# Kernel tuning notes

Measured on AMD Instinct MI355X. Metric: run time of the kernel, lower is better.

The kernel has to match this reference:

```python
import jax, jax.numpy as jnp
import numpy as np

B, S, H, D = 2, 4096, 16, 128
TILE = 128
T = S // TILE          # 32 tiles
TOPK = 7               # anchor-selected tiles per query tile (local tile appended -> 8)
DM = H * D
NEG = -1e10


def setup_inputs() -> dict:
    key = jax.random.key(0)
    ks = jax.random.split(key, 6)
    x = jax.random.normal(ks[0], (B, S, DM), dtype=jnp.float32)
    wq = jax.random.normal(ks[1], (DM, H * D), dtype=jnp.float32) * 0.02
    wk = jax.random.normal(ks[2], (DM, H * D), dtype=jnp.float32) * 0.02
    wv = jax.random.normal(ks[3], (DM, H * D), dtype=jnp.float32) * 0.02
    wo = jax.random.normal(ks[4], (H * D, DM), dtype=jnp.float32) * 0.02
    # RoPE tables (real/imag of freqs_cis), LLaMA-style
    inv_freq = 1.0 / (10000.0 ** (np.arange(0, D, 2, dtype=np.float32) / D))  # [D/2]
    t = np.arange(S, dtype=np.float32)
    freqs = np.outer(t, inv_freq)  # [S, D/2]
    cos = jnp.asarray(np.cos(freqs), dtype=jnp.float32)
    sin = jnp.asarray(np.sin(freqs), dtype=jnp.float32)
    anchor_indices = jax.random.randint(ks[5], (B, H, T, TOPK), 0, T, dtype=jnp.int32)
    return {"x": x, "wq": wq, "wk": wk, "wv": wv, "wo": wo,
            "cos": cos, "sin": sin, "anchor_indices": anchor_indices}


def _apply_rope(q, k, cos, sin):
    # q,k: [B,H,S,D]; cos,sin: [S,D/2]
    cos_f = jnp.concatenate([cos, cos], axis=-1)[None, None]  # [1,1,S,D]
    sin_f = jnp.concatenate([sin, sin], axis=-1)[None, None]

    def rot_half(x):
        h = x.shape[-1] // 2
        return jnp.concatenate([-x[..., h:], x[..., :h]], axis=-1)

    return q * cos_f + rot_half(q) * sin_f, k * cos_f + rot_half(k) * sin_f


def reference(x, wq, wk, wv, wo, cos, sin, anchor_indices):
    b, s, _ = x.shape
    h = anchor_indices.shape[1]
    t = anchor_indices.shape[2]
    tile = s // t
    d = wq.shape[1] // h

    q = (x @ wq).reshape(b, s, h, d).transpose(0, 2, 1, 3)  # [B,H,S,D]
    k = (x @ wk).reshape(b, s, h, d).transpose(0, 2, 1, 3)
    v = (x @ wv).reshape(b, s, h, d).transpose(0, 2, 1, 3)
    q, k = _apply_rope(q, k, cos, sin)

    # append local tile to anchor-selected tiles -> [B,H,T,K+1]
    local = jnp.broadcast_to(jnp.arange(t, dtype=jnp.int32)[None, None, :, None], (b, h, t, 1))
    tile_sel = jnp.concatenate([anchor_indices, local], axis=-1)
    # token indices of gathered tiles: [B,H,T,(K+1)*tile]
    offs = jnp.arange(tile, dtype=jnp.int32)[None, None, None, None, :]
    tok_idx = (tile_sel[..., None] * tile + offs)
    sparse_len = tile_sel.shape[-1] * tile
    flat_idx = jnp.clip(tok_idx.reshape(b, h, t, sparse_len), 0, s - 1)

    # gather K/V tiles: [B,H,T,L,D]
    gid = flat_idx.reshape(b, h, t * sparse_len)
    k_sp = jnp.take_along_axis(k, gid[..., None], axis=2).reshape(b, h, t, sparse_len, d)
    v_sp = jnp.take_along_axis(v, gid[..., None], axis=2).reshape(b, h, t, sparse_len, d)

    q_t = q.reshape(b, h, t, tile, d)
    logits = jnp.einsum('bhtqd,bhtkd->bhtqk', q_t, k_sp) / jnp.sqrt(jnp.float32(d))

    # causal future-mask within gathered set
    q_pos = jnp.arange(s, dtype=jnp.int32).reshape(t, tile)
    fut = flat_idx[:, :, :, None, :] > q_pos[None, None, :, :, None]  # [B,H,T,tile,L]
    logits = jnp.where(fut, NEG, logits)
    weights = jax.nn.softmax(logits, axis=-1)
    all_masked = jnp.all(fut, axis=-1, keepdims=True)
    weights = jnp.where(all_masked, 0.0, weights)
    weights = jnp.where(jnp.isnan(weights), 0.0, weights)

    out = jnp.einsum('bhtqk,bhtkd->bhtqd', weights, v_sp)
    out = out.reshape(b, h, s, d).transpose(0, 2, 1, 3).reshape(b, s, h * d)
    return out @ wo
```

## Files before the change

kernel.cpp:

```cpp
#include <hip/hip_runtime.h>
#include <hip/hip_bf16.h>


typedef __bf16 bf16_t;
using bf16x8 = __attribute__((ext_vector_type(8))) __bf16;
using bf16x4 = __attribute__((ext_vector_type(4))) __bf16;
using f32x4  = __attribute__((ext_vector_type(4))) float;

typedef const __attribute__((address_space(1))) void* gas_ptr;
typedef __attribute__((address_space(3))) void* las_ptr;

__device__ __forceinline__ void async_copy16(const void* g, void* l) {
  __builtin_amdgcn_global_load_lds((gas_ptr)g, (las_ptr)l, 16, 0, 0);
}

__device__ __forceinline__ f32x4 mfma16x16x32(bf16x8 a, bf16x8 b, f32x4 c) {
  return __builtin_amdgcn_mfma_f32_16x16x32_bf16(a, b, c, 0, 0, 0);
}

__global__ void cvt_f32_bf16(const float* __restrict__ X, bf16_t* __restrict__ Y) {
  int idx = blockIdx.x * 256 + threadIdx.x;
  float4 v = ((const float4*)X)[idx];
  bf16x4 r;
  r.x = (bf16_t)v.x; r.y = (bf16_t)v.y; r.z = (bf16_t)v.z; r.w = (bf16_t)v.w;
  ((bf16x4*)Y)[idx] = r;
}

__global__ void wtrans(const float* __restrict__ W, bf16_t* __restrict__ Wt) {
  __shared__ bf16_t t[64][66];
  const int r0 = blockIdx.x * 64, c0 = blockIdx.y * 64;
  const int tx = threadIdx.x & 63, ty = threadIdx.x >> 6;
  #pragma unroll
  for (int i = 0; i < 16; ++i) {
    int r = ty + 4 * i;
    t[r][tx] = (bf16_t)W[(size_t)(r0 + r) * 2048 + c0 + tx];
  }
  __syncthreads();
  #pragma unroll
  for (int i = 0; i < 16; ++i) {
    int n = ty + 4 * i;
    Wt[(size_t)(c0 + n) * 2048 + r0 + tx] = t[tx][n];
  }
}

__global__ __launch_bounds__(512, 2) void gemm256(
    const bf16_t* __restrict__ A, const bf16_t* __restrict__ Bt,
    int nb, int mode, float* __restrict__ Cf,
    bf16_t* __restrict__ outQ, bf16_t* __restrict__ outK,
    bf16_t* __restrict__ outVT,
    const float* __restrict__ cosT, const float* __restrict__ sinT)
{
  __shared__ bf16_t Apan[4][8192];
  __shared__ bf16_t Bpan[4][8192];
  const int bid = blockIdx.x;
  const int cpx = gridDim.x >> 3;
  const int swz = (bid & 7) * cpx + (bid >> 3);
  const int bm = (swz / nb) * 256, bn = (swz % nb) * 256;
  const int tid = threadIdx.x;
  const int w = tid >> 6, l = tid & 63;
  const int wr = w >> 1, wc = w & 1;
  const int fr = l & 15, g4 = l >> 4;

  const int c0 = tid, c1 = tid + 512;
  const int r0 = c0 >> 2, s0c = ((c0 & 3) ^ ((r0 >> 1) & 3)) * 8;
  const int r1 = c1 >> 2, s1c = ((c1 & 3) ^ ((r1 >> 1) & 3)) * 8;
  const bf16_t* aS0 = A  + (size_t)(bm + r0) * 2048 + s0c;
  const bf16_t* aS1 = A  + (size_t)(bm + r1) * 2048 + s1c;
  const bf16_t* bS0 = Bt + (size_t)(bn + r0) * 2048 + s0c;
  const bf16_t* bS1 = Bt + (size_t)(bn + r1) * 2048 + s1c;
  const int d0 = c0 * 16, d1 = c1 * 16;

  int aOff[4], bOff[8];
  #pragma unroll
  for (int m = 0; m < 4; ++m) {
    int R = wr * 64 + m * 16 + fr;
    aOff[m] = R * 64 + ((g4 ^ ((R >> 1) & 3)) << 4);
  }
  #pragma unroll
  for (int n = 0; n < 8; ++n) {
    int R = wc * 128 + n * 16 + fr;
    bOff[n] = R * 64 + ((g4 ^ ((R >> 1) & 3)) << 4);
  }

  f32x4 acc[4][8];
  #pragma unroll
  for (int m = 0; m < 4; ++m)
    #pragma unroll
    for (int n = 0; n < 8; ++n) acc[m][n] = (f32x4){0.f, 0.f, 0.f, 0.f};

  auto STAGE = [&](int phi2) {
    const int slot = phi2 & 3;
    const int kb = phi2 * 32;
    char* dA = (char*)&Apan[slot][0];
    char* dB = (char*)&Bpan[slot][0];
    async_copy16(aS0 + kb, dA + d0);
    async_copy16(aS1 + kb, dA + d1);
    async_copy16(bS0 + kb, dB + d0);
    async_copy16(bS1 + kb, dB + d1);
  };

  STAGE(0);
  STAGE(1);
  __syncthreads();

  #pragma unroll 1
  for (int phi = 0; phi < 64; ++phi) {
    const int slot = phi & 3;
    const char* pa = (const char*)&Apan[slot][0];
    const char* pb = (const char*)&Bpan[slot][0];
    bf16x8 af[4], bfr[8];
    #pragma unroll
    for (int m = 0; m < 4; ++m) af[m] = *(const bf16x8*)(pa + aOff[m]);
    #pragma unroll
    for (int n = 0; n < 8; ++n) bfr[n] = *(const bf16x8*)(pb + bOff[n]);
    if (phi < 62) {
      STAGE(phi + 2);
      asm volatile("s_waitcnt vmcnt(4)" ::: "memory");
    } else {
      asm volatile("s_waitcnt vmcnt(0)" ::: "memory");
    }
    __builtin_amdgcn_sched_barrier(0);
    __builtin_amdgcn_s_barrier();
    __builtin_amdgcn_sched_barrier(0);
    __builtin_amdgcn_s_setprio(1);
    #pragma unroll
    for (int m = 0; m < 4; ++m)
      #pragma unroll
      for (int n = 0; n < 8; ++n)
        acc[m][n] = mfma16x16x32(af[m], bfr[n], acc[m][n]);
    __builtin_amdgcn_s_setprio(0);
    __builtin_amdgcn_sched_barrier(0);
  }

  if (mode == 0) {
    #pragma unroll
    for (int m = 0; m < 4; ++m)
      #pragma unroll
      for (int n = 0; n < 8; ++n)
        #pragma unroll
        for (int j = 0; j < 4; ++j) {
          int row = bm + wr * 64 + m * 16 + g4 * 4 + j;
          int col = bn + wc * 128 + n * 16 + fr;
          Cf[(size_t)row * 2048 + col] = acc[m][n][j];
        }
    return;
  }

  const int colbase = bn + wc * 128;
  const int proj = colbase >> 11;
  const int hh = (colbase & 2047) >> 7;
  if (proj == 2) {
    #pragma unroll
    for (int m = 0; m < 4; ++m) {
      int row0 = bm + wr * 64 + m * 16 + g4 * 4;
      int b_ = row0 >> 12, sr = row0 & 4095;
      #pragma unroll
      for (int n = 0; n < 8; ++n) {
        int d_ = n * 16 + fr;
        bf16x4 pkv;
        #pragma unroll
        for (int j = 0; j < 4; ++j) pkv[j] = (bf16_t)acc[m][n][j];
        *(bf16x4*)&outVT[(((size_t)(b_ * 16 + hh)) * 128 + d_) * 4096 + sr] = pkv;
      }
    }
  } else {
    bf16_t* dst = proj ? outK : outQ;
    #pragma unroll
    for (int m = 0; m < 4; ++m) {
      int row0 = bm + wr * 64 + m * 16 + g4 * 4;
      int b_ = row0 >> 12, s0 = row0 & 4095;
      size_t hbase = ((size_t)(b_ * 16 + hh)) * 4096;
      #pragma unroll
      for (int n = 0; n < 4; ++n) {
        int d = n * 16 + fr;
        #pragma unroll
        for (int j = 0; j < 4; ++j) {
          int s = s0 + j;
          float c  = cosT[s * 64 + d];
          float sn = sinT[s * 64 + d];
          float x0 = acc[m][n][j], x1 = acc[m][n + 4][j];
          dst[(hbase + s) * 128 + d]      = (bf16_t)(x0 * c - x1 * sn);
          dst[(hbase + s) * 128 + d + 64] = (bf16_t)(x1 * c + x0 * sn);
        }
      }
    }
  }
}

__global__ __launch_bounds__(512, 4) void attn_kernel(
    const bf16_t* __restrict__ Qf, const bf16_t* __restrict__ Kf,
    const bf16_t* __restrict__ Vt, const int* __restrict__ anchors,
    bf16_t* __restrict__ outB)
{
  __shared__ bf16_t Kl[2][8192];
  __shared__ bf16_t Vl[2][8192];
  __shared__ bf16_t Pbuf[8][1024];
  const int orig = blockIdx.x;
  const int blk = (orig & 7) * 128 + (orig >> 3);
  const int qt = 31 - (blk & 31);
  const int h = (blk >> 5) & 15, b = blk >> 9;
  const int bh = b * 16 + h;
  const int tid = threadIdx.x, w = tid >> 6, l = tid & 63;
  const int fr = l & 15, g4 = l >> 4;
  const float scale = 0.08838834764831845f;

  const int* anc = anchors + ((size_t)bh * 32 + qt) * 7;
  unsigned long long pk = 0;
  int nt = 0;
  #pragma unroll
  for (int t = 0; t < 7; ++t) {
    int v = anc[t];
    if (v <= qt) { pk |= (unsigned long long)v << (5 * nt); ++nt; }
  }
  pk |= (unsigned long long)qt << (5 * nt); ++nt;
  const int NS = nt * 2;

  const bf16_t* Qbase = Qf + (size_t)bh * 4096 * 128;
  const bf16_t* Kbase = Kf + (size_t)bh * 4096 * 128;
  const bf16_t* Vbase = Vt + (size_t)bh * 128 * 4096;
  char* P = (char*)&Pbuf[w][0];

  auto STAGE = [&](int tb2, int p) {
    const bf16_t* ksrc = Kbase + (size_t)tb2 * 128;
    const bf16_t* vsrc = Vbase + tb2;
    char* kd = (char*)&Kl[p][0];
    char* vd = (char*)&Vl[p][0];
    #pragma unroll
    for (int i = 0; i < 2; ++i) {
      int c = tid + i * 512;
      int kr = c >> 4, kcol = c & 15;
      async_copy16(ksrc + (size_t)kr * 128 + (size_t)((kcol ^ (kr & 7)) * 8),
                   kd + c * 16);
      int vr = c >> 3, vcol = c & 7;
      async_copy16(vsrc + (size_t)vr * 4096 + (size_t)((vcol ^ (vr & 7)) * 8),
                   vd + c * 16);
    }
  };

  const int qrow = qt * 128 + w * 16 + fr;
  bf16x8 aq[4];
  #pragma unroll
  for (int kc = 0; kc < 4; ++kc)
    aq[kc] = *(const bf16x8*)(Qbase + (size_t)qrow * 128 + kc * 32 + g4 * 8);

  STAGE((int)(pk & 31) * 128, 0);
  __syncthreads();

  float mrun = -1e30f, lrun = 0.f;
  f32x4 o[8];
  #pragma unroll
  for (int nd = 0; nd < 8; ++nd) o[nd] = (f32x4){0.f, 0.f, 0.f, 0.f};

  for (int s = 0; s < NS; ++s) {
    const int p = s & 1;
    const int ts = (int)((pk >> (5 * (s >> 1))) & 31);
    const bool domask = (ts == qt);
    if (s + 1 < NS) {
      int s1 = s + 1;
      int ts1 = (int)((pk >> (5 * (s1 >> 1))) & 31);
      STAGE(ts1 * 128 + (s1 & 1) * 64, p ^ 1);
    }

    f32x4 sc[4];
    #pragma unroll
    for (int n = 0; n < 4; ++n) sc[n] = (f32x4){0.f, 0.f, 0.f, 0.f};
    #pragma unroll
    for (int kc = 0; kc < 4; ++kc) {
      bf16x8 kf[4];
      #pragma unroll
      for (int n = 0; n < 4; ++n) {
        int r = n * 16 + fr;
        kf[n] = *(const bf16x8*)((const char*)&Kl[p][0] +
                 r * 256 + (((kc * 4 + g4) ^ (r & 7)) << 4));
      }
      #pragma unroll
      for (int n = 0; n < 4; ++n)
        sc[n] = mfma16x16x32(kf[n], aq[kc], sc[n]);
    }

    float rmax = -1e30f;
    if (domask) {
      const int qr = w * 16 + fr;
      #pragma unroll
      for (int n = 0; n < 4; ++n)
        #pragma unroll
        for (int j = 0; j < 4; ++j) {
          float lg = sc[n][j] * scale;
          int tok = (s & 1) * 64 + n * 16 + g4 * 4 + j;
          if (tok > qr) lg = -1e10f;
          sc[n][j] = lg;
          rmax = fmaxf(rmax, lg);
        }
    } else {
      #pragma unroll
      for (int n = 0; n < 4; ++n)
        #pragma unroll
        for (int j = 0; j < 4; ++j) {
          float lg = sc[n][j] * scale;
          sc[n][j] = lg;
          rmax = fmaxf(rmax, lg);
        }
    }
    rmax = fmaxf(rmax, __shfl_xor(rmax, 16));
    rmax = fmaxf(rmax, __shfl_xor(rmax, 32));
    if (__any(rmax > mrun + 8.f)) {
      float mnew = fmaxf(mrun, rmax);
      float alpha = __expf(mrun - mnew);
      lrun *= alpha;
      #pragma unroll
      for (int nd = 0; nd < 8; ++nd)
        #pragma unroll
        for (int j = 0; j < 4; ++j) o[nd][j] *= alpha;
      mrun = mnew;
    }
    float rsum = 0.f;
    #pragma unroll
    for (int n = 0; n < 4; ++n) {
      bf16x4 pkv;
      #pragma unroll
      for (int j = 0; j < 4; ++j) {
        float pe = __expf(sc[n][j] - mrun);
        rsum += pe;
        pkv[j] = (bf16_t)pe;
      }
      int off = fr * 128 + ((((n << 1) | (g4 >> 1)) ^ (fr & 7)) << 4) + ((g4 & 1) << 3);
      *(bf16x4*)(P + off) = pkv;
    }
    rsum += __shfl_xor(rsum, 16);
    rsum += __shfl_xor(rsum, 32);
    lrun += rsum;

    #pragma unroll
    for (int kc2 = 0; kc2 < 2; ++kc2) {
      bf16x8 av[8];
      #pragma unroll
      for (int nd = 0; nd < 8; ++nd) {
        int r = nd * 16 + fr;
        av[nd] = *(const bf16x8*)((const char*)&Vl[p][0] +
                  r * 128 + (((kc2 * 4 + g4) ^ (r & 7)) << 4));
      }
      bf16x8 bp = *(const bf16x8*)(P + fr * 128 + ((((kc2 << 2) | g4) ^ (fr & 7)) << 4));
      #pragma unroll
      for (int nd = 0; nd < 8; ++nd)
        o[nd] = mfma16x16x32(av[nd], bp, o[nd]);
    }
    __syncthreads();
  }

  {
    char* E = (char*)&Kl[0][0] + w * 4096;
    float inv = 1.0f / lrun;
    #pragma unroll
    for (int nd = 0; nd < 8; ++nd) {
      bf16x4 pkv;
      #pragma unroll
      for (int j = 0; j < 4; ++j) pkv[j] = (bf16_t)(o[nd][j] * inv);
      int off = fr * 256 + ((((nd << 1) | (g4 >> 1)) ^ (fr & 7)) << 4) + ((g4 & 1) << 3);
      *(bf16x4*)(E + off) = pkv;
    }
    #pragma unroll
    for (int i = 0; i < 4; ++i) {
      int r = i * 4 + g4;
      int off = r * 256 + ((fr ^ (r & 7)) << 4);
      bf16x8 vrow = *(const bf16x8*)(E + off);
      size_t gaddr = (((size_t)b * 4096 + qt * 128 + w * 16 + r) * 2048)
                     + h * 128 + fr * 8;
      *(bf16x8*)(outB + gaddr) = vrow;
    }
  }
}

#define OFF_XB   ((size_t)0)
#define OFF_WCAT ((size_t)33554432)
#define OFF_WOT  ((size_t)58720256)
#define OFF_QF   ((size_t)67108864)
#define OFF_KF   ((size_t)100663296)
#define OFF_AT   ((size_t)134217728)
#define OFF_VT   ((size_t)167772160)

extern "C" void kernel_launch(void* const* d_in, const int* in_sizes, int n_in,
                              void* d_out, int out_size, void* d_ws, size_t ws_size,
                              hipStream_t stream) {
  (void)in_sizes; (void)n_in; (void)out_size; (void)ws_size;
  const float* x    = (const float*)d_in[0];
  const float* wq   = (const float*)d_in[1];
  const float* wk   = (const float*)d_in[2];
  const float* wv   = (const float*)d_in[3];
  const float* wo   = (const float*)d_in[4];
  const float* cosT = (const float*)d_in[5];
  const float* sinT = (const float*)d_in[6];
  const int*   anc  = (const int*)d_in[7];
  float* out = (float*)d_out;
  char* ws = (char*)d_ws;

  bf16_t* xb   = (bf16_t*)(ws + OFF_XB);
  bf16_t* wcat = (bf16_t*)(ws + OFF_WCAT);
  bf16_t* wqt  = wcat;
  bf16_t* wkt  = wcat + (size_t)2048 * 2048;
  bf16_t* wvt  = wcat + (size_t)4096 * 2048;
  bf16_t* wot  = (bf16_t*)(ws + OFF_WOT);
  bf16_t* Qf   = (bf16_t*)(ws + OFF_QF);
  bf16_t* Kf   = (bf16_t*)(ws + OFF_KF);
  bf16_t* Vt   = (bf16_t*)(ws + OFF_VT);
  bf16_t* attnB = (bf16_t*)(ws + OFF_AT);

  cvt_f32_bf16<<<16384, 256, 0, stream>>>(x, xb);
  wtrans<<<dim3(32, 32), 256, 0, stream>>>(wq, wqt);
  wtrans<<<dim3(32, 32), 256, 0, stream>>>(wk, wkt);
  wtrans<<<dim3(32, 32), 256, 0, stream>>>(wv, wvt);
  wtrans<<<dim3(32, 32), 256, 0, stream>>>(wo, wot);
  gemm256<<<768, 512, 0, stream>>>(xb, wcat, 24, 1, nullptr, Qf, Kf, Vt, cosT, sinT);
  attn_kernel<<<1024, 512, 0, stream>>>(Qf, Kf, Vt, anc, attnB);
  gemm256<<<256, 512, 0, stream>>>(attnB, wot, 8, 0, out, nullptr, nullptr, nullptr,
                                   nullptr, nullptr);
}
```

Before: 382.4 us.

## Restructure GEMM main loop into split A/B staging with finer barriers

The GEMM main loop now processes two K-slices per iteration, split into four half-steps. Each half-step issues A or B async loads separately and interleaves LDS fragment reads with MFMA groups under extra barriers, with the prefetch depth raised to three stages. The block-to-tile swizzle is changed to group blocks by row for better L2 reuse, and the four weight transposes are merged into one launch. The finer-grained barriers add synchronization overhead in exchange for better overlap of loads and compute.

```diff
diff --git a/kernel.cpp b/kernel.cpp
--- a/kernel.cpp
+++ b/kernel.cpp
@@ -17,6 +17,8 @@
 __device__ __forceinline__ f32x4 mfma16x16x32(bf16x8 a, bf16x8 b, f32x4 c) {
   return __builtin_amdgcn_mfma_f32_16x16x32_bf16(a, b, c, 0, 0, 0);
 }
+
+#define SBAR0() __builtin_amdgcn_sched_barrier(0)
 
 __global__ void cvt_f32_bf16(const float* __restrict__ X, bf16_t* __restrict__ Y) {
   int idx = blockIdx.x * 256 + threadIdx.x;
@@ -26,8 +28,13 @@
   ((bf16x4*)Y)[idx] = r;
 }
 
-__global__ void wtrans(const float* __restrict__ W, bf16_t* __restrict__ Wt) {
+__global__ void wtrans4(const float* __restrict__ wq, const float* __restrict__ wk,
+                        const float* __restrict__ wv, const float* __restrict__ wo,
+                        bf16_t* __restrict__ wcat, bf16_t* __restrict__ wot) {
   __shared__ bf16_t t[64][66];
+  const int z = blockIdx.z;
+  const float* W = (z == 0) ? wq : (z == 1) ? wk : (z == 2) ? wv : wo;
+  bf16_t* Wt = (z == 3) ? wot : (wcat + (size_t)z * 2048 * 2048);
   const int r0 = blockIdx.x * 64, c0 = blockIdx.y * 64;
   const int tx = threadIdx.x & 63, ty = threadIdx.x >> 6;
   #pragma unroll
@@ -55,19 +62,21 @@
   const int bid = blockIdx.x;
   const int cpx = gridDim.x >> 3;
   const int swz = (bid & 7) * cpx + (bid >> 3);
-  const int bm = (swz / nb) * 256, bn = (swz % nb) * 256;
+  const int RM = cpx / nb;
+  const int bm = ((swz / cpx) * RM + (swz % RM)) * 256;
+  const int bn = ((swz % cpx) / RM) * 256;
   const int tid = threadIdx.x;
   const int w = tid >> 6, l = tid & 63;
   const int wr = w >> 1, wc = w & 1;
   const int fr = l & 15, g4 = l >> 4;
 
   const int c0 = tid, c1 = tid + 512;
-  const int r0 = c0 >> 2, s0c = ((c0 & 3) ^ ((r0 >> 1) & 3)) * 8;
-  const int r1 = c1 >> 2, s1c = ((c1 & 3) ^ ((r1 >> 1) & 3)) * 8;
-  const bf16_t* aS0 = A  + (size_t)(bm + r0) * 2048 + s0c;
-  const bf16_t* aS1 = A  + (size_t)(bm + r1) * 2048 + s1c;
-  const bf16_t* bS0 = Bt + (size_t)(bn + r0) * 2048 + s0c;
-  const bf16_t* bS1 = Bt + (size_t)(bn + r1) * 2048 + s1c;
+  const int r0 = c0 >> 2, ch0 = c0 & 3;
+  const int r1 = c1 >> 2, ch1 = c1 & 3;
+  const bf16_t* aS0 = A  + (size_t)(bm + r0) * 2048 + (ch0 ^ ((r0 >> 1) & 3)) * 8;
+  const bf16_t* aS1 = A  + (size_t)(bm + r1) * 2048 + (ch1 ^ ((r1 >> 1) & 3)) * 8;
+  const bf16_t* bS0 = Bt + (size_t)(bn + r0) * 2048 + (ch0 ^ ((r0 >> 1) & 3)) * 8;
+  const bf16_t* bS1 = Bt + (size_t)(bn + r1) * 2048 + (ch1 ^ ((r1 >> 1) & 3)) * 8;
   const int d0 = c0 * 16, d1 = c1 * 16;
 
   int aOff[4], bOff[8];
@@ -88,48 +97,100 @@
     #pragma unroll
     for (int n = 0; n < 8; ++n) acc[m][n] = (f32x4){0.f, 0.f, 0.f, 0.f};
 
-  auto STAGE = [&](int phi2) {
-    const int slot = phi2 & 3;
-    const int kb = phi2 * 32;
+  auto STAGE_A = [&](int H) {
+    const int slot = H & 3;
+    const int kb = (H >> 1) * 64 + (H & 1) * 32;
     char* dA = (char*)&Apan[slot][0];
-    char* dB = (char*)&Bpan[slot][0];
     async_copy16(aS0 + kb, dA + d0);
     async_copy16(aS1 + kb, dA + d1);
+  };
+  auto STAGE_B = [&](int H) {
+    const int slot = H & 3;
+    const int kb = (H >> 1) * 64 + (H & 1) * 32;
+    char* dB = (char*)&Bpan[slot][0];
     async_copy16(bS0 + kb, dB + d0);
     async_copy16(bS1 + kb, dB + d1);
   };
 
-  STAGE(0);
-  STAGE(1);
-  __syncthreads();
+  STAGE_A(0); STAGE_B(0); STAGE_A(1); STAGE_B(1); STAGE_A(2); STAGE_B(2);
+  asm volatile("s_waitcnt vmcnt(4)" ::: "memory");
+  SBAR0();
+  __builtin_amdgcn_s_barrier();
+  SBAR0();
 
   #pragma unroll 1
-  for (int phi = 0; phi < 64; ++phi) {
-    const int slot = phi & 3;
-    const char* pa = (const char*)&Apan[slot][0];
-    const char* pb = (const char*)&Bpan[slot][0];
-    bf16x8 af[4], bfr[8];
-    #pragma unroll
-    for (int m = 0; m < 4; ++m) af[m] = *(const bf16x8*)(pa + aOff[m]);
-    #pragma unroll
-    for (int n = 0; n < 8; ++n) bfr[n] = *(const bf16x8*)(pb + bOff[n]);
-    if (phi < 62) {
-      STAGE(phi + 2);
-      asm volatile("s_waitcnt vmcnt(4)" ::: "memory");
-    } else {
-      asm volatile("s_waitcnt vmcnt(0)" ::: "memory");
-    }
-    __builtin_amdgcn_sched_barrier(0);
-    __builtin_amdgcn_s_barrier();
-    __builtin_amdgcn_sched_barrier(0);
+  for (int t = 0; t < 32; ++t) {
+    const char* pa0 = (const char*)&Apan[(2 * t) & 3][0];
+    const char* pb0 = (const char*)&Bpan[(2 * t) & 3][0];
+    const char* pa1 = (const char*)&Apan[(2 * t + 1) & 3][0];
+    const char* pb1 = (const char*)&Bpan[(2 * t + 1) & 3][0];
+    bf16x8 bq[8], a0, a1;
+
+    a0 = *(const bf16x8*)(pa0 + aOff[0]);
+    a1 = *(const bf16x8*)(pa0 + aOff[1]);
+    #pragma unroll
+    for (int n = 0; n < 8; ++n) bq[n] = *(const bf16x8*)(pb0 + bOff[n]);
+    if (t < 31) STAGE_A(2 * t + 3);
+    SBAR0(); __builtin_amdgcn_s_barrier();
+    asm volatile("s_waitcnt lgkmcnt(0)" ::: "memory");
+    SBAR0();
     __builtin_amdgcn_s_setprio(1);
     #pragma unroll
-    for (int m = 0; m < 4; ++m)
-      #pragma unroll
-      for (int n = 0; n < 8; ++n)
-        acc[m][n] = mfma16x16x32(af[m], bfr[n], acc[m][n]);
+    for (int n = 0; n < 8; ++n) {
+      acc[0][n] = mfma16x16x32(a0, bq[n], acc[0][n]);
+      acc[1][n] = mfma16x16x32(a1, bq[n], acc[1][n]);
+    }
     __builtin_amdgcn_s_setprio(0);
-    __builtin_amdgcn_sched_barrier(0);
+    SBAR0(); __builtin_amdgcn_s_barrier(); SBAR0();
+
+    a0 = *(const bf16x8*)(pa0 + aOff[2]);
+    a1 = *(const bf16x8*)(pa0 + aOff[3]);
+    if (t < 31) STAGE_B(2 * t + 3);
+    SBAR0(); __builtin_amdgcn_s_barrier();
+    asm volatile("s_waitcnt lgkmcnt(0)" ::: "memory");
+    SBAR0();
+    __builtin_amdgcn_s_setprio(1);
+    #pragma unroll
+    for (int n = 0; n < 8; ++n) {
+      acc[2][n] = mfma16x16x32(a0, bq[n], acc[2][n]);
+      acc[3][n] = mfma16x16x32(a1, bq[n], acc[3][n]);
+    }
+    __builtin_amdgcn_s_setprio(0);
+    SBAR0(); __builtin_amdgcn_s_barrier(); SBAR0();
+
+    a0 = *(const bf16x8*)(pa1 + aOff[0]);
+    a1 = *(const bf16x8*)(pa1 + aOff[1]);
+    #pragma unroll
+    for (int n = 0; n < 8; ++n) bq[n] = *(const bf16x8*)(pb1 + bOff[n]);
+    if (t < 30) STAGE_A(2 * t + 4);
+    SBAR0(); __builtin_amdgcn_s_barrier();
+    asm volatile("s_waitcnt lgkmcnt(0)" ::: "memory");
+    SBAR0();
+    __builtin_amdgcn_s_setprio(1);
+    #pragma unroll
+    for (int n = 0; n < 8; ++n) {
+      acc[0][n] = mfma16x16x32(a0, bq[n], acc[0][n]);
+      acc[1][n] = mfma16x16x32(a1, bq[n], acc[1][n]);
+    }
+    __builtin_amdgcn_s_setprio(0);
+    SBAR0(); __builtin_amdgcn_s_barrier(); SBAR0();
+
+    a0 = *(const bf16x8*)(pa1 + aOff[2]);
+    a1 = *(const bf16x8*)(pa1 + aOff[3]);
+    if (t < 30) STAGE_B(2 * t + 4);
+    SBAR0(); __builtin_amdgcn_s_barrier();
+    asm volatile("s_waitcnt lgkmcnt(0)" ::: "memory");
+    SBAR0();
+    __builtin_amdgcn_s_setprio(1);
+    #pragma unroll
+    for (int n = 0; n < 8; ++n) {
+      acc[2][n] = mfma16x16x32(a0, bq[n], acc[2][n]);
+      acc[3][n] = mfma16x16x32(a1, bq[n], acc[3][n]);
+    }
+    __builtin_amdgcn_s_setprio(0);
+    if (t < 30)       asm volatile("s_waitcnt vmcnt(4)" ::: "memory");
+    else if (t == 30) asm volatile("s_waitcnt vmcnt(0)" ::: "memory");
+    SBAR0(); __builtin_amdgcn_s_barrier(); SBAR0();
   }
 
   if (mode == 0) {
@@ -164,7 +225,7 @@
       }
     }
   } else {
-    bf16_t* dst = proj ? outK : outQ;
+    bf16_t* dst_ = proj ? outK : outQ;
     #pragma unroll
     for (int m = 0; m < 4; ++m) {
       int row0 = bm + wr * 64 + m * 16 + g4 * 4;
@@ -179,8 +240,8 @@
           float c  = cosT[s * 64 + d];
           float sn = sinT[s * 64 + d];
           float x0 = acc[m][n][j], x1 = acc[m][n + 4][j];
-          dst[(hbase + s) * 128 + d]      = (bf16_t)(x0 * c - x1 * sn);
-          dst[(hbase + s) * 128 + d + 64] = (bf16_t)(x1 * c + x0 * sn);
+          dst_[(hbase + s) * 128 + d]      = (bf16_t)(x0 * c - x1 * sn);
+          dst_[(hbase + s) * 128 + d + 64] = (bf16_t)(x1 * c + x0 * sn);
         }
       }
     }
@@ -395,9 +456,6 @@
 
   bf16_t* xb   = (bf16_t*)(ws + OFF_XB);
   bf16_t* wcat = (bf16_t*)(ws + OFF_WCAT);
-  bf16_t* wqt  = wcat;
-  bf16_t* wkt  = wcat + (size_t)2048 * 2048;
-  bf16_t* wvt  = wcat + (size_t)4096 * 2048;
   bf16_t* wot  = (bf16_t*)(ws + OFF_WOT);
   bf16_t* Qf   = (bf16_t*)(ws + OFF_QF);
   bf16_t* Kf   = (bf16_t*)(ws + OFF_KF);
@@ -405,10 +463,7 @@
   bf16_t* attnB = (bf16_t*)(ws + OFF_AT);
 
   cvt_f32_bf16<<<16384, 256, 0, stream>>>(x, xb);
-  wtrans<<<dim3(32, 32), 256, 0, stream>>>(wq, wqt);
-  wtrans<<<dim3(32, 32), 256, 0, stream>>>(wk, wkt);
-  wtrans<<<dim3(32, 32), 256, 0, stream>>>(wv, wvt);
-  wtrans<<<dim3(32, 32), 256, 0, stream>>>(wo, wot);
+  wtrans4<<<dim3(32, 32, 4), 256, 0, stream>>>(wq, wk, wv, wo, wcat, wot);
   gemm256<<<768, 512, 0, stream>>>(xb, wcat, 24, 1, nullptr, Qf, Kf, Vt, cosT, sinT);
   attn_kernel<<<1024, 512, 0, stream>>>(Qf, Kf, Vt, anc, attnB);
   gemm256<<<256, 512, 0, stream>>>(attnB, wot, 8, 0, out, nullptr, nullptr, nullptr,
```

Result: no change. 385.6 us (+0.8%).
